# Kernel optimization log

Measured on AMD Instinct MI355X. Metric: run time of the kernel, lower is better.

Reference implementation:

```python
import jax, jax.numpy as jnp
import numpy as np

NEG_BIG = -1e9


def setup_inputs() -> dict:
    key = jax.random.key(0)
    kq, kk, kv, km = jax.random.split(key, 4)
    B, H, S, D = 2, 16, 2048, 64
    query = jax.random.normal(kq, (B, H, S, D), dtype=jnp.float32)
    k = jax.random.normal(kk, (B, H, S, D), dtype=jnp.float32)
    value = jax.random.normal(kv, (B, H, S, D), dtype=jnp.float32)
    attention_mask = jax.random.randint(km, (B, 1, S, S), 0, 2, dtype=jnp.int32)
    return {"query": query, "key": k, "value": value, "attention_mask": attention_mask}


def reference(query, key, value, attention_mask):
    d_k = query.shape[-1]
    scale = 1.0 / jnp.sqrt(jnp.float32(d_k))
    # [B,H,S,S] scores (module materializes full score matrix)
    scores = jnp.einsum('bhqd,bhkd->bhqk', query, key) * scale
    scores = scores + attention_mask.astype(scores.dtype) * NEG_BIG
    probs = jax.nn.softmax(scores, axis=-1)
    out = jnp.einsum('bhqk,bhkd->bhqd', probs, value)
    return out
```

## Files before the change

### kernel.cpp

```cpp
#include <hip/hip_runtime.h>

#define NB 2
#define NH 16
#define SEQ 2048
#define DH 64
#define SC 0.125f
#define NEGB (-1e9f)

typedef __bf16 bf16x8 __attribute__((ext_vector_type(8)));
typedef unsigned short u16x8 __attribute__((ext_vector_type(8)));
typedef unsigned short u16x4 __attribute__((ext_vector_type(4)));
typedef float f32x4 __attribute__((ext_vector_type(4)));
typedef unsigned long long u64;

#if __has_builtin(__builtin_amdgcn_exp2f)
#define EXP2F __builtin_amdgcn_exp2f
#else
#define EXP2F exp2f
#endif

__device__ __forceinline__ unsigned short f2b(float f) {
    unsigned u = __builtin_bit_cast(unsigned, f);
    u += 0x7fffu + ((u >> 16) & 1u);
    return (unsigned short)(u >> 16);
}
__device__ __forceinline__ unsigned short f2b_rh(float f) {
    return (unsigned short)((__builtin_bit_cast(unsigned, f) + 0x8000u) >> 16);
}

template<int CTRL>
__device__ __forceinline__ float dppf(float x) {
    int i = __builtin_bit_cast(int, x);
    return __builtin_bit_cast(float, __builtin_amdgcn_update_dpp(i, i, CTRL, 0xF, 0xF, false));
}
__device__ __forceinline__ float rowmax16(float v) {
    v = fmaxf(v, dppf<0xB1>(v));
    v = fmaxf(v, dppf<0x4E>(v));
    v = fmaxf(v, dppf<0x141>(v));
    v = fmaxf(v, dppf<0x140>(v));
    return v;
}
__device__ __forceinline__ float rowsum16(float v) {
    v += dppf<0xB1>(v);
    v += dppf<0x4E>(v);
    v += dppf<0x141>(v);
    v += dppf<0x140>(v);
    return v;
}


__global__ void conv_qk(const float* __restrict__ Q, const float* __restrict__ K,
                        unsigned short* __restrict__ Qb, unsigned short* __restrict__ Kb,
                        int n8) {
    int i = blockIdx.x * blockDim.x + threadIdx.x;
    int stride = gridDim.x * blockDim.x;
    for (int j = i; j < n8; j += stride) {
        float4 a = ((const float4*)Q)[j * 2];
        float4 b = ((const float4*)Q)[j * 2 + 1];
        u16x8 u;
        u[0]=f2b(a.x); u[1]=f2b(a.y); u[2]=f2b(a.z); u[3]=f2b(a.w);
        u[4]=f2b(b.x); u[5]=f2b(b.y); u[6]=f2b(b.z); u[7]=f2b(b.w);
        ((u16x8*)Qb)[j] = u;
    }
    for (int j = i; j < n8; j += stride) {
        float4 a = ((const float4*)K)[j * 2];
        float4 b = ((const float4*)K)[j * 2 + 1];
        u16x8 u;
        u[0]=f2b(a.x); u[1]=f2b(a.y); u[2]=f2b(a.z); u[3]=f2b(a.w);
        u[4]=f2b(b.x); u[5]=f2b(b.y); u[6]=f2b(b.z); u[7]=f2b(b.w);
        ((u16x8*)Kb)[j] = u;
    }
}

__global__ __launch_bounds__(256) void transpose_v(const float* __restrict__ V,
                                                   unsigned short* __restrict__ Vt) {
    __shared__ __align__(16) unsigned short t[64][72];
    const int tid = threadIdx.x;
    const int bh = blockIdx.x >> 5;
    const int kt = blockIdx.x & 31;
    const float* src = V + (size_t)bh * SEQ * DH + (size_t)kt * 64 * DH;
    {
        int r = tid >> 2, c0 = (tid & 3) * 16;
        #pragma unroll
        for (int j = 0; j < 4; ++j) {
            float4 a = *(const float4*)(src + r * DH + c0 + j * 4);
            u16x4 u;
            u[0]=f2b(a.x); u[1]=f2b(a.y); u[2]=f2b(a.z); u[3]=f2b(a.w);
            *(u16x4*)&t[r][c0 + j * 4] = u;
        }
    }
    __syncthreads();
    {
        int d = tid >> 2, k0 = (tid & 3) * 16;
        unsigned short* dst = Vt + (size_t)bh * DH * SEQ + (size_t)d * SEQ + (size_t)kt * 64 + k0;
        u16x8 w0, w1;
        #pragma unroll
        for (int j = 0; j < 8; ++j) { w0[j] = t[k0 + j][d]; w1[j] = t[k0 + 8 + j][d]; }
        *(u16x8*)dst = w0;
        *(u16x8*)(dst + 8) = w1;
    }
}

__global__ void pack_mask(const int* __restrict__ mask, u64* __restrict__ words, int nwords) {
    int wv = (blockIdx.x * blockDim.x + threadIdx.x) >> 6;
    int lane = threadIdx.x & 63;
    int nwv = (gridDim.x * blockDim.x) >> 6;
    for (int w0 = wv * 4; w0 < nwords; w0 += nwv * 4) {
        int m0 = mask[(size_t)w0 * 64 + lane];
        int m1 = mask[(size_t)(w0 + 1) * 64 + lane];
        int m2 = mask[(size_t)(w0 + 2) * 64 + lane];
        int m3 = mask[(size_t)(w0 + 3) * 64 + lane];
        u64 b0 = __ballot(m0 != 0), b1 = __ballot(m1 != 0);
        u64 b2 = __ballot(m2 != 0), b3 = __ballot(m3 != 0);
        if (lane == 0) { words[w0] = b0; words[w0+1] = b1; words[w0+2] = b2; words[w0+3] = b3; }
    }
}

__global__ __launch_bounds__(512, 6)
void attn_fwd3(const unsigned short* __restrict__ Qb, const unsigned short* __restrict__ Kb,
               const unsigned short* __restrict__ Vtb, const u64* __restrict__ mw,
               float* __restrict__ Og)
{
    __shared__ __align__(16) unsigned short K_lds[2][64][64];
    __shared__ __align__(16) unsigned short V_lds[2][64][64];
    __shared__ __align__(16) unsigned short P_lds[8][16][72];

    const int tid  = threadIdx.x;
    const int wid  = tid >> 6;
    const int lane = tid & 63;
    const int l15  = lane & 15;
    const int g    = lane >> 4;

    const int bid  = blockIdx.x;
    const int slot = bid >> 3;
    const int bh   = (bid & 7) + 8 * (slot >> 4);
    const int qt   = slot & 15;
    const int b    = bh >> 4;

    const size_t base = (size_t)bh * SEQ * DH;
    const unsigned short* Kbh = Kb + base;
    const unsigned short* Vbh = Vtb + base;

    bf16x8 qf[2];
    {
        const unsigned short* qp = Qb + base + (size_t)(qt * 128 + wid * 16 + l15) * DH + g * 8;
        qf[0] = __builtin_bit_cast(bf16x8, *(const u16x8*)qp);
        qf[1] = __builtin_bit_cast(bf16x8, *(const u16x8*)(qp + 32));
    }

    const int q_r0 = qt * 128 + wid * 16 + g * 4;
    const u64* mrow = mw + (size_t)b * SEQ * (SEQ / 64);

    const int sr = wid * 8 + (lane >> 3);
    const int sc_ = (((lane & 7) ^ (sr & 7)) * 8);
    const unsigned short* Ksrc0 = Kbh + (size_t)sr * DH + sc_;
    const unsigned short* Vsrc0 = Vbh + (size_t)sr * SEQ + sc_;
    unsigned short* KdstA = &K_lds[0][0][0] + (size_t)(wid * 64 + lane) * 8;
    unsigned short* KdstB = &K_lds[1][0][0] + (size_t)(wid * 64 + lane) * 8;
    unsigned short* VdstA = &V_lds[0][0][0] + (size_t)(wid * 64 + lane) * 8;
    unsigned short* VdstB = &V_lds[1][0][0] + (size_t)(wid * 64 + lane) * 8;

    u16x8 kreg, vreg;
    #define STAGE_LOAD(t) { const int kv0_ = (t) * 64; \
        kreg = *(const u16x8*)(Ksrc0 + (size_t)kv0_ * DH); \
        vreg = *(const u16x8*)(Vsrc0 + kv0_); }
    #define STAGE_WRITE(bf) { \
        *(u16x8*)((bf) ? KdstB : KdstA) = kreg; \
        *(u16x8*)((bf) ? VdstB : VdstA) = vreg; }

    u16x8 ou;
    #pragma unroll
    for (int j = 0; j < 8; ++j) ou[j] = 0x3F80;
    const bf16x8 onesb = __builtin_bit_cast(bf16x8, ou);

    f32x4 oacc[4];
    #pragma unroll
    for (int dt = 0; dt < 4; ++dt) oacc[dt] = (f32x4){0.f, 0.f, 0.f, 0.f};
    f32x4 lacc = (f32x4){0.f, 0.f, 0.f, 0.f};

    u64 w_cur[4], w_nxt[4];
    #pragma unroll
    for (int r = 0; r < 4; ++r) w_cur[r] = mrow[(size_t)(q_r0 + r) * (SEQ / 64)];
    STAGE_LOAD(0); STAGE_WRITE(0);
    __syncthreads();

    const float KSC = 0.18033688f;
    const float KB  = -11.54156509f;

    for (int it = 0; it < SEQ / 64; ++it) {
        const int cur = it & 1;
        const bool more = (it + 1 < SEQ / 64);
        if (more) {
            STAGE_LOAD(it + 1);
            #pragma unroll
            for (int r = 0; r < 4; ++r)
                w_nxt[r] = mrow[(size_t)(q_r0 + r) * (SEQ / 64) + it + 1];
        }

        f32x4 sacc[4];
        #pragma unroll
        for (int r = 0; r < 4; ++r) {
            u64 x = w_cur[r] >> l15;
            sacc[0][r] = (x & 1ull)         ? NEGB : 0.f;
            sacc[1][r] = ((x >> 16) & 1ull) ? NEGB : 0.f;
            sacc[2][r] = ((x >> 32) & 1ull) ? NEGB : 0.f;
            sacc[3][r] = ((x >> 48) & 1ull) ? NEGB : 0.f;
        }
        #pragma unroll
        for (int kt = 0; kt < 2; ++kt) {
            #pragma unroll
            for (int ct = 0; ct < 4; ++ct) {
                const int row = ct * 16 + l15;
                u16x8 ku = *(const u16x8*)(&K_lds[cur][0][0] + row * 64 + (((kt * 4 + g) ^ (row & 7)) * 8));
                sacc[ct] = __builtin_amdgcn_mfma_f32_16x16x32_bf16(
                    qf[kt], __builtin_bit_cast(bf16x8, ku), sacc[ct], 0, 0, 0);
            }
        }

        #pragma unroll
        for (int ct = 0; ct < 4; ++ct)
            #pragma unroll
            for (int r = 0; r < 4; ++r) {
                float p = EXP2F(fmaf(sacc[ct][r], KSC, KB));
                P_lds[wid][g * 4 + r][ct * 16 + l15] = f2b_rh(p);
            }

        #pragma unroll
        for (int kt = 0; kt < 2; ++kt) {
            u16x8 pu = *(const u16x8*)&P_lds[wid][l15][kt * 32 + g * 8];
            bf16x8 pa = __builtin_bit_cast(bf16x8, pu);
            lacc = __builtin_amdgcn_mfma_f32_16x16x32_bf16(pa, onesb, lacc, 0, 0, 0);
            #pragma unroll
            for (int dt = 0; dt < 4; ++dt) {
                const int row = dt * 16 + l15;
                u16x8 vu = *(const u16x8*)(&V_lds[cur][0][0] + row * 64 + (((kt * 4 + g) ^ (row & 7)) * 8));
                oacc[dt] = __builtin_amdgcn_mfma_f32_16x16x32_bf16(
                    pa, __builtin_bit_cast(bf16x8, vu), oacc[dt], 0, 0, 0);
            }
        }

        if (more) {
            STAGE_WRITE(cur ^ 1);
            #pragma unroll
            for (int r = 0; r < 4; ++r) w_cur[r] = w_nxt[r];
        }
        __syncthreads();
    }

    float inv[4];
    #pragma unroll
    for (int r = 0; r < 4; ++r) inv[r] = 1.0f / lacc[r];
    #pragma unroll
    for (int dt = 0; dt < 4; ++dt)
        #pragma unroll
        for (int r = 0; r < 4; ++r)
            Og[base + (size_t)(q_r0 + r) * DH + dt * 16 + l15] = oacc[dt][r] * inv[r];
    #undef STAGE_LOAD
    #undef STAGE_WRITE
}

__global__ __launch_bounds__(256, 2)
void attn_fwd_fb(const float* __restrict__ Qg, const float* __restrict__ Kg,
                 const float* __restrict__ Vg, const int* __restrict__ maskg,
                 float* __restrict__ Og)
{
    __shared__ unsigned short Klds[64][72];
    __shared__ unsigned short Vt[64][72];
    __shared__ unsigned short Plds[4][16][72];

    const int tid  = threadIdx.x;
    const int wid  = tid >> 6;
    const int lane = tid & 63;
    const int l15  = lane & 15;
    const int g    = lane >> 4;

    const int bh    = blockIdx.x >> 5;
    const int qtile = blockIdx.x & 31;
    const int b     = bh >> 4;
    const size_t base = (size_t)bh * SEQ * DH;

    bf16x8 qf[2];
    {
        const int qrow = qtile * 64 + wid * 16 + l15;
        const float* qp = Qg + base + (size_t)qrow * DH + g * 8;
        #pragma unroll
        for (int kt = 0; kt < 2; ++kt) {
            float4 a = *(const float4*)(qp + kt * 32);
            float4 c = *(const float4*)(qp + kt * 32 + 4);
            u16x8 u;
            u[0]=f2b(a.x); u[1]=f2b(a.y); u[2]=f2b(a.z); u[3]=f2b(a.w);
            u[4]=f2b(c.x); u[5]=f2b(c.y); u[6]=f2b(c.z); u[7]=f2b(c.w);
            qf[kt] = __builtin_bit_cast(bf16x8, u);
        }
    }

    float m_r[4], l_r[4];
    f32x4 oacc[4];
    #pragma unroll
    for (int r = 0; r < 4; ++r) { m_r[r] = -3.0e38f; l_r[r] = 0.f; }
    #pragma unroll
    for (int dt = 0; dt < 4; ++dt) oacc[dt] = (f32x4){0.f, 0.f, 0.f, 0.f};

    const int q_r0 = qtile * 64 + wid * 16 + g * 4;

    for (int it = 0; it < SEQ / 64; ++it) {
        const int kvbase = it * 64;
        __syncthreads();
        #pragma unroll
        for (int i = 0; i < 4; ++i) {
            int f4  = i * 256 + tid;
            int row = f4 >> 4;
            int c4  = f4 & 15;
            float4 kk = *(const float4*)(Kg + base + (size_t)(kvbase + row) * DH + c4 * 4);
            u16x4 kb;
            kb[0]=f2b(kk.x); kb[1]=f2b(kk.y); kb[2]=f2b(kk.z); kb[3]=f2b(kk.w);
            *(u16x4*)&Klds[row][c4 * 4] = kb;
        }
        {
            const float* vp = Vg + base + (size_t)(kvbase + wid * 16) * DH + lane;
            #pragma unroll
            for (int i = 0; i < 4; ++i) {
                u16x4 vv;
                #pragma unroll
                for (int k = 0; k < 4; ++k)
                    vv[k] = f2b(vp[(i * 4 + k) * DH]);
                *(u16x4*)&Vt[lane][wid * 16 + i * 4] = vv;
            }
        }
        __syncthreads();

        f32x4 sacc[4];
        #pragma unroll
        for (int ct = 0; ct < 4; ++ct) sacc[ct] = (f32x4){0.f, 0.f, 0.f, 0.f};
        #pragma unroll
        for (int kt = 0; kt < 2; ++kt) {
            #pragma unroll
            for (int ct = 0; ct < 4; ++ct) {
                u16x8 ku = *(const u16x8*)&Klds[ct * 16 + l15][kt * 32 + g * 8];
                sacc[ct] = __builtin_amdgcn_mfma_f32_16x16x32_bf16(
                    qf[kt], __builtin_bit_cast(bf16x8, ku), sacc[ct], 0, 0, 0);
            }
        }

        float sc[4][4];
        #pragma unroll
        for (int ct = 0; ct < 4; ++ct)
            #pragma unroll
            for (int r = 0; r < 4; ++r) {
                float s = sacc[ct][r] * SC;
                int mv = maskg[((size_t)b * SEQ + (q_r0 + r)) * SEQ + kvbase + ct * 16 + l15];
                sc[ct][r] = s + (float)mv * NEGB;
            }

        #pragma unroll
        for (int r = 0; r < 4; ++r) {
            float mxv = fmaxf(fmaxf(sc[0][r], sc[1][r]), fmaxf(sc[2][r], sc[3][r]));
            mxv = rowmax16(mxv);
            float mnew = fmaxf(m_r[r], mxv);
            float corr = __expf(m_r[r] - mnew);
            m_r[r] = mnew;
            float psum = 0.f;
            #pragma unroll
            for (int ct = 0; ct < 4; ++ct) {
                float p = __expf(sc[ct][r] - mnew);
                sc[ct][r] = p;
                psum += p;
            }
            psum = rowsum16(psum);
            l_r[r] = l_r[r] * corr + psum;
            #pragma unroll
            for (int dt = 0; dt < 4; ++dt) oacc[dt][r] *= corr;
        }

        #pragma unroll
        for (int ct = 0; ct < 4; ++ct)
            #pragma unroll
            for (int r = 0; r < 4; ++r)
                Plds[wid][g * 4 + r][ct * 16 + l15] = f2b(sc[ct][r]);

        #pragma unroll
        for (int kt = 0; kt < 2; ++kt) {
            u16x8 pu = *(const u16x8*)&Plds[wid][l15][kt * 32 + g * 8];
            bf16x8 pa = __builtin_bit_cast(bf16x8, pu);
            #pragma unroll
            for (int dt = 0; dt < 4; ++dt) {
                u16x8 vu = *(const u16x8*)&Vt[dt * 16 + l15][kt * 32 + g * 8];
                oacc[dt] = __builtin_amdgcn_mfma_f32_16x16x32_bf16(
                    pa, __builtin_bit_cast(bf16x8, vu), oacc[dt], 0, 0, 0);
            }
        }
    }

    #pragma unroll
    for (int dt = 0; dt < 4; ++dt)
        #pragma unroll
        for (int r = 0; r < 4; ++r) {
            int q = q_r0 + r;
            Og[base + (size_t)q * DH + dt * 16 + l15] = oacc[dt][r] / l_r[r];
        }
}

extern "C" void kernel_launch(void* const* d_in, const int* in_sizes, int n_in,
                              void* d_out, int out_size, void* d_ws, size_t ws_size,
                              hipStream_t stream) {
    const float* Q = (const float*)d_in[0];
    const float* K = (const float*)d_in[1];
    const float* V = (const float*)d_in[2];
    const int* mask = (const int*)d_in[3];
    float* out = (float*)d_out;

    const size_t nelem   = (size_t)NB * NH * SEQ * DH;
    const size_t bfBytes = nelem * 2;
    const int    nwords  = NB * SEQ * (SEQ / 64);
    const size_t wBytes  = (size_t)nwords * 8;

    const size_t offQ = 0, offK = bfBytes, offV = 2 * bfBytes, offW = 3 * bfBytes;
    const size_t needFull = 3 * bfBytes + wBytes;

    if (ws_size >= needFull) {
        unsigned short* Qb  = (unsigned short*)((char*)d_ws + offQ);
        unsigned short* Kb  = (unsigned short*)((char*)d_ws + offK);
        unsigned short* Vtb = (unsigned short*)((char*)d_ws + offV);
        u64*            mwp = (u64*)((char*)d_ws + offW);

        conv_qk<<<2048, 256, 0, stream>>>(Q, K, Qb, Kb, (int)(nelem / 8));
        transpose_v<<<NB * NH * (SEQ / 64), 256, 0, stream>>>(V, Vtb);
        pack_mask<<<1024, 256, 0, stream>>>(mask, mwp, nwords);
        attn_fwd3<<<512, 512, 0, stream>>>(Qb, Kb, Vtb, mwp, out);
    } else {
        attn_fwd_fb<<<NB * NH * (SEQ / 64), 256, 0, stream>>>(Q, K, V, mask, out);
    }
}
```

Baseline: 183.1 us.

## Give each wave 32 query rows and pack P pairs with a permuted V layout

The attention kernel moves to 4 waves per block, each owning two 16-row query tiles. Every K and V fragment read from LDS now feeds two MFMAs, halving LDS reads per unit of math. Probabilities are packed two-per-dword with a byte permute into a permuted column order, and transpose_v reorders V's key dimension to match, cutting LDS store instructions. In exchange, register pressure rises and the mask words are loaded inside the loop instead of being prefetched one iteration ahead, which may expose global-load latency.

```diff
diff --git a/kernel.cpp b/kernel.cpp
--- a/kernel.cpp
+++ b/kernel.cpp
@@ -10,6 +10,7 @@
 typedef __bf16 bf16x8 __attribute__((ext_vector_type(8)));
 typedef unsigned short u16x8 __attribute__((ext_vector_type(8)));
 typedef unsigned short u16x4 __attribute__((ext_vector_type(4)));
+typedef unsigned u32x4 __attribute__((ext_vector_type(4)));
 typedef float f32x4 __attribute__((ext_vector_type(4)));
 typedef unsigned long long u64;
 
@@ -24,8 +25,11 @@
     u += 0x7fffu + ((u >> 16) & 1u);
     return (unsigned short)(u >> 16);
 }
-__device__ __forceinline__ unsigned short f2b_rh(float f) {
-    return (unsigned short)((__builtin_bit_cast(unsigned, f) + 0x8000u) >> 16);
+
+__device__ __forceinline__ unsigned pack2_bf16(float a, float b) {
+    unsigned ua = __builtin_bit_cast(unsigned, a) + 0x8000u;
+    unsigned ub = __builtin_bit_cast(unsigned, b) + 0x8000u;
+    return __builtin_amdgcn_perm(ub, ua, 0x07060302u);
 }
 
 template<int CTRL>
@@ -72,6 +76,10 @@
     }
 }
 
+__device__ __forceinline__ int pi_inv(int c) {
+    return ((c >> 5) << 5) | ((c & 1) << 4) | ((c >> 1) & 15);
+}
+
 __global__ __launch_bounds__(256) void transpose_v(const float* __restrict__ V,
                                                    unsigned short* __restrict__ Vt) {
     __shared__ __align__(16) unsigned short t[64][72];
@@ -95,7 +103,10 @@
         unsigned short* dst = Vt + (size_t)bh * DH * SEQ + (size_t)d * SEQ + (size_t)kt * 64 + k0;
         u16x8 w0, w1;
         #pragma unroll
-        for (int j = 0; j < 8; ++j) { w0[j] = t[k0 + j][d]; w1[j] = t[k0 + 8 + j][d]; }
+        for (int j = 0; j < 8; ++j) {
+            w0[j] = t[pi_inv(k0 + j)][d];
+            w1[j] = t[pi_inv(k0 + 8 + j)][d];
+        }
         *(u16x8*)dst = w0;
         *(u16x8*)(dst + 8) = w1;
     }
@@ -116,14 +127,14 @@
     }
 }
 
-__global__ __launch_bounds__(512, 6)
-void attn_fwd3(const unsigned short* __restrict__ Qb, const unsigned short* __restrict__ Kb,
+__global__ __launch_bounds__(256, 3)
+void attn_fwd5(const unsigned short* __restrict__ Qb, const unsigned short* __restrict__ Kb,
                const unsigned short* __restrict__ Vtb, const u64* __restrict__ mw,
                float* __restrict__ Og)
 {
     __shared__ __align__(16) unsigned short K_lds[2][64][64];
     __shared__ __align__(16) unsigned short V_lds[2][64][64];
-    __shared__ __align__(16) unsigned short P_lds[8][16][72];
+    __shared__ __align__(16) unsigned P_lds[4][32][36];
 
     const int tid  = threadIdx.x;
     const int wid  = tid >> 6;
@@ -141,46 +152,51 @@
     const unsigned short* Kbh = Kb + base;
     const unsigned short* Vbh = Vtb + base;
 
-    bf16x8 qf[2];
-    {
-        const unsigned short* qp = Qb + base + (size_t)(qt * 128 + wid * 16 + l15) * DH + g * 8;
-        qf[0] = __builtin_bit_cast(bf16x8, *(const u16x8*)qp);
-        qf[1] = __builtin_bit_cast(bf16x8, *(const u16x8*)(qp + 32));
-    }
-
-    const int q_r0 = qt * 128 + wid * 16 + g * 4;
-    const u64* mrow = mw + (size_t)b * SEQ * (SEQ / 64);
-
-    const int sr = wid * 8 + (lane >> 3);
-    const int sc_ = (((lane & 7) ^ (sr & 7)) * 8);
-    const unsigned short* Ksrc0 = Kbh + (size_t)sr * DH + sc_;
-    const unsigned short* Vsrc0 = Vbh + (size_t)sr * SEQ + sc_;
-    unsigned short* KdstA = &K_lds[0][0][0] + (size_t)(wid * 64 + lane) * 8;
-    unsigned short* KdstB = &K_lds[1][0][0] + (size_t)(wid * 64 + lane) * 8;
-    unsigned short* VdstA = &V_lds[0][0][0] + (size_t)(wid * 64 + lane) * 8;
-    unsigned short* VdstB = &V_lds[1][0][0] + (size_t)(wid * 64 + lane) * 8;
-
-    u16x8 kreg, vreg;
+    bf16x8 qf[2][2];
+    #pragma unroll
+    for (int a = 0; a < 2; ++a) {
+        const unsigned short* qp = Qb + base + (size_t)(qt * 128 + wid * 32 + a * 16 + l15) * DH + g * 8;
+        qf[a][0] = __builtin_bit_cast(bf16x8, *(const u16x8*)qp);
+        qf[a][1] = __builtin_bit_cast(bf16x8, *(const u16x8*)(qp + 32));
+    }
+
+    const u64* mp = mw + ((size_t)b * SEQ + qt * 128 + wid * 32 + g * 4) * (SEQ / 64);
+
+    const int sr = tid >> 3;
+    const int scc = (((tid & 7) ^ (sr & 7)) * 8);
+    const unsigned short* Ksrc = Kbh + (size_t)sr * DH + scc;
+    const unsigned short* Vsrc = Vbh + (size_t)sr * SEQ + scc;
+    unsigned short* const Kdst0 = &K_lds[0][0][0] + (size_t)tid * 8;
+    unsigned short* const Kdst1 = &K_lds[1][0][0] + (size_t)tid * 8;
+    unsigned short* const Vdst0 = &V_lds[0][0][0] + (size_t)tid * 8;
+    unsigned short* const Vdst1 = &V_lds[1][0][0] + (size_t)tid * 8;
+
+    u16x8 kr0, kr1, vr0, vr1;
     #define STAGE_LOAD(t) { const int kv0_ = (t) * 64; \
-        kreg = *(const u16x8*)(Ksrc0 + (size_t)kv0_ * DH); \
-        vreg = *(const u16x8*)(Vsrc0 + kv0_); }
+        kr0 = *(const u16x8*)(Ksrc + (size_t)kv0_ * DH); \
+        kr1 = *(const u16x8*)(Ksrc + (size_t)(kv0_ + 32) * DH); \
+        vr0 = *(const u16x8*)(Vsrc + kv0_); \
+        vr1 = *(const u16x8*)(Vsrc + (size_t)32 * SEQ + kv0_); }
     #define STAGE_WRITE(bf) { \
-        *(u16x8*)((bf) ? KdstB : KdstA) = kreg; \
-        *(u16x8*)((bf) ? VdstB : VdstA) = vreg; }
+        unsigned short* kd_ = (bf) ? Kdst1 : Kdst0; \
+        unsigned short* vd_ = (bf) ? Vdst1 : Vdst0; \
+        *(u16x8*)kd_ = kr0; *(u16x8*)(kd_ + 2048) = kr1; \
+        *(u16x8*)vd_ = vr0; *(u16x8*)(vd_ + 2048) = vr1; }
 
     u16x8 ou;
     #pragma unroll
     for (int j = 0; j < 8; ++j) ou[j] = 0x3F80;
     const bf16x8 onesb = __builtin_bit_cast(bf16x8, ou);
 
-    f32x4 oacc[4];
-    #pragma unroll
-    for (int dt = 0; dt < 4; ++dt) oacc[dt] = (f32x4){0.f, 0.f, 0.f, 0.f};
-    f32x4 lacc = (f32x4){0.f, 0.f, 0.f, 0.f};
-
-    u64 w_cur[4], w_nxt[4];
-    #pragma unroll
-    for (int r = 0; r < 4; ++r) w_cur[r] = mrow[(size_t)(q_r0 + r) * (SEQ / 64)];
+    f32x4 oacc[2][4];
+    #pragma unroll
+    for (int a = 0; a < 2; ++a)
+        #pragma unroll
+        for (int dt = 0; dt < 4; ++dt) oacc[a][dt] = (f32x4){0.f, 0.f, 0.f, 0.f};
+    f32x4 lacc[2];
+    lacc[0] = (f32x4){0.f, 0.f, 0.f, 0.f};
+    lacc[1] = (f32x4){0.f, 0.f, 0.f, 0.f};
+
     STAGE_LOAD(0); STAGE_WRITE(0);
     __syncthreads();
 
@@ -190,71 +206,78 @@
     for (int it = 0; it < SEQ / 64; ++it) {
         const int cur = it & 1;
         const bool more = (it + 1 < SEQ / 64);
-        if (more) {
-            STAGE_LOAD(it + 1);
-            #pragma unroll
-            for (int r = 0; r < 4; ++r)
-                w_nxt[r] = mrow[(size_t)(q_r0 + r) * (SEQ / 64) + it + 1];
-        }
-
-        f32x4 sacc[4];
-        #pragma unroll
-        for (int r = 0; r < 4; ++r) {
-            u64 x = w_cur[r] >> l15;
-            sacc[0][r] = (x & 1ull)         ? NEGB : 0.f;
-            sacc[1][r] = ((x >> 16) & 1ull) ? NEGB : 0.f;
-            sacc[2][r] = ((x >> 32) & 1ull) ? NEGB : 0.f;
-            sacc[3][r] = ((x >> 48) & 1ull) ? NEGB : 0.f;
-        }
+        if (more) STAGE_LOAD(it + 1);
+
+        f32x4 sacc[2][4];
+        #pragma unroll
+        for (int a = 0; a < 2; ++a)
+            #pragma unroll
+            for (int r = 0; r < 4; ++r) {
+                u64 x = mp[(size_t)(a * 16 + r) * (SEQ / 64) + it] >> l15;
+                sacc[a][0][r] = (x & 1ull)         ? NEGB : 0.f;
+                sacc[a][1][r] = ((x >> 16) & 1ull) ? NEGB : 0.f;
+                sacc[a][2][r] = ((x >> 32) & 1ull) ? NEGB : 0.f;
+                sacc[a][3][r] = ((x >> 48) & 1ull) ? NEGB : 0.f;
+            }
         #pragma unroll
         for (int kt = 0; kt < 2; ++kt) {
             #pragma unroll
             for (int ct = 0; ct < 4; ++ct) {
                 const int row = ct * 16 + l15;
                 u16x8 ku = *(const u16x8*)(&K_lds[cur][0][0] + row * 64 + (((kt * 4 + g) ^ (row & 7)) * 8));
-                sacc[ct] = __builtin_amdgcn_mfma_f32_16x16x32_bf16(
-                    qf[kt], __builtin_bit_cast(bf16x8, ku), sacc[ct], 0, 0, 0);
-            }
-        }
-
-        #pragma unroll
-        for (int ct = 0; ct < 4; ++ct)
+                bf16x8 kb = __builtin_bit_cast(bf16x8, ku);
+                sacc[0][ct] = __builtin_amdgcn_mfma_f32_16x16x32_bf16(qf[0][kt], kb, sacc[0][ct], 0, 0, 0);
+                sacc[1][ct] = __builtin_amdgcn_mfma_f32_16x16x32_bf16(qf[1][kt], kb, sacc[1][ct], 0, 0, 0);
+            }
+        }
+
+        #pragma unroll
+        for (int a = 0; a < 2; ++a)
             #pragma unroll
             for (int r = 0; r < 4; ++r) {
-                float p = EXP2F(fmaf(sacc[ct][r], KSC, KB));
-                P_lds[wid][g * 4 + r][ct * 16 + l15] = f2b_rh(p);
+                float p0 = EXP2F(fmaf(sacc[a][0][r], KSC, KB));
+                float p1 = EXP2F(fmaf(sacc[a][1][r], KSC, KB));
+                float p2 = EXP2F(fmaf(sacc[a][2][r], KSC, KB));
+                float p3 = EXP2F(fmaf(sacc[a][3][r], KSC, KB));
+                const int row = a * 16 + g * 4 + r;
+                P_lds[wid][row][l15]      = pack2_bf16(p0, p1);
+                P_lds[wid][row][16 + l15] = pack2_bf16(p2, p3);
             }
 
         #pragma unroll
         for (int kt = 0; kt < 2; ++kt) {
-            u16x8 pu = *(const u16x8*)&P_lds[wid][l15][kt * 32 + g * 8];
-            bf16x8 pa = __builtin_bit_cast(bf16x8, pu);
-            lacc = __builtin_amdgcn_mfma_f32_16x16x32_bf16(pa, onesb, lacc, 0, 0, 0);
+            u32x4 pu0 = *(const u32x4*)&P_lds[wid][l15][kt * 16 + g * 4];
+            u32x4 pu1 = *(const u32x4*)&P_lds[wid][16 + l15][kt * 16 + g * 4];
+            bf16x8 pa0 = __builtin_bit_cast(bf16x8, pu0);
+            bf16x8 pa1 = __builtin_bit_cast(bf16x8, pu1);
+            lacc[0] = __builtin_amdgcn_mfma_f32_16x16x32_bf16(pa0, onesb, lacc[0], 0, 0, 0);
+            lacc[1] = __builtin_amdgcn_mfma_f32_16x16x32_bf16(pa1, onesb, lacc[1], 0, 0, 0);
             #pragma unroll
             for (int dt = 0; dt < 4; ++dt) {
                 const int row = dt * 16 + l15;
                 u16x8 vu = *(const u16x8*)(&V_lds[cur][0][0] + row * 64 + (((kt * 4 + g) ^ (row & 7)) * 8));
-                oacc[dt] = __builtin_amdgcn_mfma_f32_16x16x32_bf16(
-                    pa, __builtin_bit_cast(bf16x8, vu), oacc[dt], 0, 0, 0);
-            }
-        }
-
-        if (more) {
-            STAGE_WRITE(cur ^ 1);
-            #pragma unroll
-            for (int r = 0; r < 4; ++r) w_cur[r] = w_nxt[r];
-        }
+                bf16x8 vb = __builtin_bit_cast(bf16x8, vu);
+                oacc[0][dt] = __builtin_amdgcn_mfma_f32_16x16x32_bf16(pa0, vb, oacc[0][dt], 0, 0, 0);
+                oacc[1][dt] = __builtin_amdgcn_mfma_f32_16x16x32_bf16(pa1, vb, oacc[1][dt], 0, 0, 0);
+            }
+        }
+
+        if (more) STAGE_WRITE(cur ^ 1);
         __syncthreads();
     }
 
-    float inv[4];
-    #pragma unroll
-    for (int r = 0; r < 4; ++r) inv[r] = 1.0f / lacc[r];
-    #pragma unroll
-    for (int dt = 0; dt < 4; ++dt)
-        #pragma unroll
-        for (int r = 0; r < 4; ++r)
-            Og[base + (size_t)(q_r0 + r) * DH + dt * 16 + l15] = oacc[dt][r] * inv[r];
+    #pragma unroll
+    for (int a = 0; a < 2; ++a) {
+        float inv[4];
+        #pragma unroll
+        for (int r = 0; r < 4; ++r) inv[r] = 1.0f / lacc[a][r];
+        const int q0 = qt * 128 + wid * 32 + a * 16 + g * 4;
+        #pragma unroll
+        for (int dt = 0; dt < 4; ++dt)
+            #pragma unroll
+            for (int r = 0; r < 4; ++r)
+                Og[base + (size_t)(q0 + r) * DH + dt * 16 + l15] = oacc[a][dt][r] * inv[r];
+    }
     #undef STAGE_LOAD
     #undef STAGE_WRITE
 }
@@ -426,7 +449,7 @@
         conv_qk<<<2048, 256, 0, stream>>>(Q, K, Qb, Kb, (int)(nelem / 8));
         transpose_v<<<NB * NH * (SEQ / 64), 256, 0, stream>>>(V, Vtb);
         pack_mask<<<1024, 256, 0, stream>>>(mask, mwp, nwords);
-        attn_fwd3<<<512, 512, 0, stream>>>(Qb, Kb, Vtb, mwp, out);
+        attn_fwd5<<<512, 256, 0, stream>>>(Qb, Kb, Vtb, mwp, out);
     } else {
         attn_fwd_fb<<<NB * NH * (SEQ / 64), 256, 0, stream>>>(Q, K, V, mask, out);
     }
```

Measured after the change: 206.9 us. 13.0% more time.

## Fuse Q bf16 conversion into attention kernel, pack P pairs, permute V

Applied to the files above, without the earlier changes.

Drops the separate Q conversion pass: each wave now loads its fp32 Q rows directly and converts them to bf16 in registers. Probabilities are packed two per 32-bit LDS word, so four exps produce two stores instead of four 16-bit stores. To keep the PV MFMA operand order correct, V's key dimension is permuted during the transpose. It also adds s_setprio around the MFMA blocks to favour matrix issue, at the cost of added layout coupling between kernels.

```diff
diff --git a/kernel.cpp b/kernel.cpp
--- a/kernel.cpp
+++ b/kernel.cpp
@@ -10,6 +10,7 @@
 typedef __bf16 bf16x8 __attribute__((ext_vector_type(8)));
 typedef unsigned short u16x8 __attribute__((ext_vector_type(8)));
 typedef unsigned short u16x4 __attribute__((ext_vector_type(4)));
+typedef unsigned u32x4 __attribute__((ext_vector_type(4)));
 typedef float f32x4 __attribute__((ext_vector_type(4)));
 typedef unsigned long long u64;
 
@@ -24,8 +25,11 @@
     u += 0x7fffu + ((u >> 16) & 1u);
     return (unsigned short)(u >> 16);
 }
-__device__ __forceinline__ unsigned short f2b_rh(float f) {
-    return (unsigned short)((__builtin_bit_cast(unsigned, f) + 0x8000u) >> 16);
+
+__device__ __forceinline__ unsigned pack2_bf16(float a, float b) {
+    unsigned ua = __builtin_bit_cast(unsigned, a) + 0x8000u;
+    unsigned ub = __builtin_bit_cast(unsigned, b) + 0x8000u;
+    return __builtin_amdgcn_perm(ub, ua, 0x07060302u);
 }
 
 template<int CTRL>
@@ -49,19 +53,9 @@
 }
 
 
-__global__ void conv_qk(const float* __restrict__ Q, const float* __restrict__ K,
-                        unsigned short* __restrict__ Qb, unsigned short* __restrict__ Kb,
-                        int n8) {
+__global__ void conv_k(const float* __restrict__ K, unsigned short* __restrict__ Kb, int n8) {
     int i = blockIdx.x * blockDim.x + threadIdx.x;
     int stride = gridDim.x * blockDim.x;
-    for (int j = i; j < n8; j += stride) {
-        float4 a = ((const float4*)Q)[j * 2];
-        float4 b = ((const float4*)Q)[j * 2 + 1];
-        u16x8 u;
-        u[0]=f2b(a.x); u[1]=f2b(a.y); u[2]=f2b(a.z); u[3]=f2b(a.w);
-        u[4]=f2b(b.x); u[5]=f2b(b.y); u[6]=f2b(b.z); u[7]=f2b(b.w);
-        ((u16x8*)Qb)[j] = u;
-    }
     for (int j = i; j < n8; j += stride) {
         float4 a = ((const float4*)K)[j * 2];
         float4 b = ((const float4*)K)[j * 2 + 1];
@@ -70,6 +64,10 @@
         u[4]=f2b(b.x); u[5]=f2b(b.y); u[6]=f2b(b.z); u[7]=f2b(b.w);
         ((u16x8*)Kb)[j] = u;
     }
+}
+
+__device__ __forceinline__ int pi_inv(int c) {
+    return ((c >> 5) << 5) | ((c & 1) << 4) | ((c >> 1) & 15);
 }
 
 __global__ __launch_bounds__(256) void transpose_v(const float* __restrict__ V,
@@ -95,7 +93,10 @@
         unsigned short* dst = Vt + (size_t)bh * DH * SEQ + (size_t)d * SEQ + (size_t)kt * 64 + k0;
         u16x8 w0, w1;
         #pragma unroll
-        for (int j = 0; j < 8; ++j) { w0[j] = t[k0 + j][d]; w1[j] = t[k0 + 8 + j][d]; }
+        for (int j = 0; j < 8; ++j) {
+            w0[j] = t[pi_inv(k0 + j)][d];
+            w1[j] = t[pi_inv(k0 + 8 + j)][d];
+        }
         *(u16x8*)dst = w0;
         *(u16x8*)(dst + 8) = w1;
     }
@@ -117,13 +118,13 @@
 }
 
 __global__ __launch_bounds__(512, 6)
-void attn_fwd3(const unsigned short* __restrict__ Qb, const unsigned short* __restrict__ Kb,
+void attn_fwd6(const float* __restrict__ Qg, const unsigned short* __restrict__ Kb,
                const unsigned short* __restrict__ Vtb, const u64* __restrict__ mw,
                float* __restrict__ Og)
 {
     __shared__ __align__(16) unsigned short K_lds[2][64][64];
     __shared__ __align__(16) unsigned short V_lds[2][64][64];
-    __shared__ __align__(16) unsigned short P_lds[8][16][72];
+    __shared__ __align__(16) unsigned P_lds[8][16][36];
 
     const int tid  = threadIdx.x;
     const int wid  = tid >> 6;
@@ -143,9 +144,16 @@
 
     bf16x8 qf[2];
     {
-        const unsigned short* qp = Qb + base + (size_t)(qt * 128 + wid * 16 + l15) * DH + g * 8;
-        qf[0] = __builtin_bit_cast(bf16x8, *(const u16x8*)qp);
-        qf[1] = __builtin_bit_cast(bf16x8, *(const u16x8*)(qp + 32));
+        const float* qp = Qg + base + (size_t)(qt * 128 + wid * 16 + l15) * DH + g * 8;
+        #pragma unroll
+        for (int kt = 0; kt < 2; ++kt) {
+            float4 a = *(const float4*)(qp + kt * 32);
+            float4 c = *(const float4*)(qp + kt * 32 + 4);
+            u16x8 u;
+            u[0]=f2b(a.x); u[1]=f2b(a.y); u[2]=f2b(a.z); u[3]=f2b(a.w);
+            u[4]=f2b(c.x); u[5]=f2b(c.y); u[6]=f2b(c.z); u[7]=f2b(c.w);
+            qf[kt] = __builtin_bit_cast(bf16x8, u);
+        }
     }
 
     const int q_r0 = qt * 128 + wid * 16 + g * 4;
@@ -155,18 +163,20 @@
     const int sc_ = (((lane & 7) ^ (sr & 7)) * 8);
     const unsigned short* Ksrc0 = Kbh + (size_t)sr * DH + sc_;
     const unsigned short* Vsrc0 = Vbh + (size_t)sr * SEQ + sc_;
-    unsigned short* KdstA = &K_lds[0][0][0] + (size_t)(wid * 64 + lane) * 8;
-    unsigned short* KdstB = &K_lds[1][0][0] + (size_t)(wid * 64 + lane) * 8;
-    unsigned short* VdstA = &V_lds[0][0][0] + (size_t)(wid * 64 + lane) * 8;
-    unsigned short* VdstB = &V_lds[1][0][0] + (size_t)(wid * 64 + lane) * 8;
+    unsigned short* const KdstA = &K_lds[0][0][0] + (size_t)(wid * 64 + lane) * 8;
+    unsigned short* const KdstB = &K_lds[1][0][0] + (size_t)(wid * 64 + lane) * 8;
+    unsigned short* const VdstA = &V_lds[0][0][0] + (size_t)(wid * 64 + lane) * 8;
+    unsigned short* const VdstB = &V_lds[1][0][0] + (size_t)(wid * 64 + lane) * 8;
 
     u16x8 kreg, vreg;
     #define STAGE_LOAD(t) { const int kv0_ = (t) * 64; \
         kreg = *(const u16x8*)(Ksrc0 + (size_t)kv0_ * DH); \
         vreg = *(const u16x8*)(Vsrc0 + kv0_); }
     #define STAGE_WRITE(bf) { \
-        *(u16x8*)((bf) ? KdstB : KdstA) = kreg; \
-        *(u16x8*)((bf) ? VdstB : VdstA) = vreg; }
+        unsigned short* kd_ = (bf) ? KdstB : KdstA; \
+        unsigned short* vd_ = (bf) ? VdstB : VdstA; \
+        *(u16x8*)kd_ = kreg; \
+        *(u16x8*)vd_ = vreg; }
 
     u16x8 ou;
     #pragma unroll
@@ -206,6 +216,7 @@
             sacc[2][r] = ((x >> 32) & 1ull) ? NEGB : 0.f;
             sacc[3][r] = ((x >> 48) & 1ull) ? NEGB : 0.f;
         }
+        __builtin_amdgcn_s_setprio(1);
         #pragma unroll
         for (int kt = 0; kt < 2; ++kt) {
             #pragma unroll
@@ -216,19 +227,24 @@
                     qf[kt], __builtin_bit_cast(bf16x8, ku), sacc[ct], 0, 0, 0);
             }
         }
-
-        #pragma unroll
-        for (int ct = 0; ct < 4; ++ct)
-            #pragma unroll
-            for (int r = 0; r < 4; ++r) {
-                float p = EXP2F(fmaf(sacc[ct][r], KSC, KB));
-                P_lds[wid][g * 4 + r][ct * 16 + l15] = f2b_rh(p);
-            }
-
-        #pragma unroll
-        for (int kt = 0; kt < 2; ++kt) {
-            u16x8 pu = *(const u16x8*)&P_lds[wid][l15][kt * 32 + g * 8];
+        __builtin_amdgcn_s_setprio(0);
+
+        #pragma unroll
+        for (int r = 0; r < 4; ++r) {
+            float p0 = EXP2F(fmaf(sacc[0][r], KSC, KB));
+            float p1 = EXP2F(fmaf(sacc[1][r], KSC, KB));
+            float p2 = EXP2F(fmaf(sacc[2][r], KSC, KB));
+            float p3 = EXP2F(fmaf(sacc[3][r], KSC, KB));
+            const int row = g * 4 + r;
+            P_lds[wid][row][l15]      = pack2_bf16(p0, p1);
+            P_lds[wid][row][16 + l15] = pack2_bf16(p2, p3);
+        }
+
+        #pragma unroll
+        for (int kt = 0; kt < 2; ++kt) {
+            u32x4 pu = *(const u32x4*)&P_lds[wid][l15][kt * 16 + g * 4];
             bf16x8 pa = __builtin_bit_cast(bf16x8, pu);
+            __builtin_amdgcn_s_setprio(1);
             lacc = __builtin_amdgcn_mfma_f32_16x16x32_bf16(pa, onesb, lacc, 0, 0, 0);
             #pragma unroll
             for (int dt = 0; dt < 4; ++dt) {
@@ -237,6 +253,7 @@
                 oacc[dt] = __builtin_amdgcn_mfma_f32_16x16x32_bf16(
                     pa, __builtin_bit_cast(bf16x8, vu), oacc[dt], 0, 0, 0);
             }
+            __builtin_amdgcn_s_setprio(0);
         }
 
         if (more) {
@@ -414,19 +431,18 @@
     const int    nwords  = NB * SEQ * (SEQ / 64);
     const size_t wBytes  = (size_t)nwords * 8;
 
-    const size_t offQ = 0, offK = bfBytes, offV = 2 * bfBytes, offW = 3 * bfBytes;
-    const size_t needFull = 3 * bfBytes + wBytes;
+    const size_t offK = 0, offV = bfBytes, offW = 2 * bfBytes;
+    const size_t needFull = 2 * bfBytes + wBytes;
 
     if (ws_size >= needFull) {
-        unsigned short* Qb  = (unsigned short*)((char*)d_ws + offQ);
         unsigned short* Kb  = (unsigned short*)((char*)d_ws + offK);
         unsigned short* Vtb = (unsigned short*)((char*)d_ws + offV);
         u64*            mwp = (u64*)((char*)d_ws + offW);
 
-        conv_qk<<<2048, 256, 0, stream>>>(Q, K, Qb, Kb, (int)(nelem / 8));
+        conv_k<<<1024, 256, 0, stream>>>(K, Kb, (int)(nelem / 8));
         transpose_v<<<NB * NH * (SEQ / 64), 256, 0, stream>>>(V, Vtb);
         pack_mask<<<1024, 256, 0, stream>>>(mask, mwp, nwords);
-        attn_fwd3<<<512, 512, 0, stream>>>(Qb, Kb, Vtb, mwp, out);
+        attn_fwd6<<<512, 512, 0, stream>>>(Q, Kb, Vtb, mwp, out);
     } else {
         attn_fwd_fb<<<NB * NH * (SEQ / 64), 256, 0, stream>>>(Q, K, V, mask, out);
     }
```

Result: slower. 190.2 us (+3.9%).
